# Optimization experiments

Measured on AMD Instinct MI355X. Metric: run time of the kernel, lower is better.

## Reference

```python
import jax, jax.numpy as jnp
import numpy as np

L = 3          # n_layers
B = 512        # batch
H = 1024       # d_model == d_enopt (last-layer hidden is fed back as input)
T = 8          # num_targets
TAU = 96       # decode steps
BETA = 2.0     # softplus beta


def setup_inputs() -> dict:
    key = jax.random.key(0)
    ks = jax.random.split(key, 10)
    s = 0.02
    return {
        "hidden": jax.random.normal(ks[0], (L, B, H), jnp.float32),
        "cell":   jax.random.normal(ks[1], (L, B, H), jnp.float32),
        # stacked per-layer LSTM weights (input size == H for all layers)
        "W_ih": jax.random.normal(ks[2], (L, 4 * H, H), jnp.float32) * s,
        "W_hh": jax.random.normal(ks[3], (L, 4 * H, H), jnp.float32) * s,
        "b_ih": jax.random.normal(ks[4], (L, 4 * H), jnp.float32) * s,
        "b_hh": jax.random.normal(ks[5], (L, 4 * H), jnp.float32) * s,
        "W1": jax.random.normal(ks[6], (T, H), jnp.float32) * s,
        "b1": jax.random.normal(ks[7], (T,), jnp.float32) * s,
        "W2": jax.random.normal(ks[8], (T, H), jnp.float32) * s,
        "b2": jax.random.normal(ks[9], (T,), jnp.float32) * s,
    }


def _lstm_step(h, c, W_ih, W_hh, b_ih, b_hh):
    x = h[-1]  # [B, H]
    new_h, new_c = [], []
    for l in range(L):
        gates = x @ W_ih[l].T + b_ih[l] + h[l] @ W_hh[l].T + b_hh[l]  # [B, 4H]
        i, f, g, o = jnp.split(gates, 4, axis=-1)  # PyTorch gate order i,f,g,o
        i, f, o = jax.nn.sigmoid(i), jax.nn.sigmoid(f), jax.nn.sigmoid(o)
        g = jnp.tanh(g)
        c_l = f * c[l] + i * g
        h_l = o * jnp.tanh(c_l)
        new_h.append(h_l)
        new_c.append(c_l)
        x = h_l  # input to next layer (dropout inactive at inference)
    return jnp.stack(new_h), jnp.stack(new_c), x


def reference(hidden, cell, W_ih, W_hh, b_ih, b_hh, W1, b1, W2, b2):
    def step(carry, _):
        h, c = carry
        h, c, y = _lstm_step(h, c, W_ih, W_hh, b_ih, b_hh)
        return (h, c), y

    (_, _), ys = jax.lax.scan(step, (hidden, cell), None, length=TAU)  # ys: [TAU, B, H]
    out = jnp.transpose(ys, (1, 0, 2))  # [B, TAU, H] (batch_first concat over time)
    mu = out @ W1.T + b1
    sigma = jax.nn.softplus(BETA * (out @ W2.T + b2)) / BETA
    return mu, sigma
```

## Files before the change

kernel.cpp:

```cpp
#include <hip/hip_runtime.h>
#include <hip/hip_bf16.h>
#include <stdint.h>


typedef __attribute__((ext_vector_type(8))) short short8;
typedef __attribute__((ext_vector_type(8))) __bf16 bf16x8_t;
typedef __attribute__((ext_vector_type(4))) float f32x4;
typedef __attribute__((ext_vector_type(4))) unsigned short u16x4;

static __device__ __forceinline__ unsigned short f2bf(float f) {
  unsigned int u = __float_as_uint(f);
  u += 0x7FFFu + ((u >> 16) & 1u);
  return (unsigned short)(u >> 16);
}

static __device__ __forceinline__ float sigm(float x) {
  return 1.0f / (1.0f + __expf(-x));
}
static __device__ __forceinline__ float tanh_f(float x) {
  float xc = fminf(fmaxf(x, -15.f), 15.f);
  float e = __expf(2.0f * xc);
  return 1.0f - 2.0f / (e + 1.0f);
}

static __device__ __forceinline__ void gload_lds16(const void* g, void* l) {
  __builtin_amdgcn_global_load_lds(
      (const __attribute__((address_space(1))) unsigned int*)g,
      (__attribute__((address_space(3))) unsigned int*)l, 16, 0, 0);
}

static __device__ __forceinline__ f32x4 mfma16(short8 a, short8 b, f32x4 c) {
  return __builtin_amdgcn_mfma_f32_16x16x32_bf16((bf16x8_t)a, (bf16x8_t)b, c, 0, 0, 0);
}

__global__ __launch_bounds__(256, 1) void phase_kernel(
    const unsigned short* __restrict__ Wx,
    const unsigned short* __restrict__ xsrc,
    const float* __restrict__ gb_rd,
    float* __restrict__ c_l,
    unsigned short* __restrict__ h_out,
    const float* __restrict__ bias_l,
    int do_proj, int step, float* __restrict__ macc,
    const float* __restrict__ W1, const float* __restrict__ W2,
    const unsigned short* __restrict__ Wh,
    const unsigned short* __restrict__ hsrc,
    float* __restrict__ gb_wr,
    int do_x, int do_h) {
  __shared__ __align__(16) char ldsA[2][32768];

  const int bi = blockIdx.x;
  const int xcd = bi & 7;
  const int rslot = bi >> 3;
  const int pair = xcd * 4 + (rslot >> 3);
  const int mt = rslot & 7;
  const int role = pair & 1;
  const int hcg = pair >> 1;
  const int tile = hcg * 8 + mt;
  const int m0 = mt * 64;
  const int hc0 = hcg * 64;

  if (role == 0) { if (!do_x) return; } else { if (!do_h) return; }

  const unsigned short* A = role ? hsrc : xsrc;
  const unsigned short* W = role ? Wh : Wx;

  const int tid = threadIdx.x;
  const int w = tid >> 6;
  const int lane = tid & 63;
  const int quad = lane >> 4;
  const int l16 = lane & 15;

  const unsigned short* brow[4];
#pragma unroll
  for (int g = 0; g < 4; ++g)
    brow[g] = W + (size_t)(g * 1024 + hc0 + w * 16 + l16) * 1024 + quad * 8;

  const int rbase = tid >> 5;
  const int spos = tid & 31;
  const int wvbase = (tid >> 6) * 1024;

  const int rx0 = l16, rx1 = 16 + l16;

#define STAGE(kc_, buf_)                                                      \
  {                                                                           \
    _Pragma("unroll") for (int j = 0; j < 8; ++j) {                           \
      int r_ = j * 8 + rbase;                                                 \
      int c_ = spos ^ (r_ & 31);                                              \
      gload_lds16(A + (size_t)(m0 + r_) * 1024 + (kc_)*256 + c_ * 8,          \
                  &ldsA[buf_][j * 4096 + wvbase]);                            \
    }                                                                         \
  }

  STAGE(0, 0);
  short8 bfr[4][4];
#pragma unroll
  for (int d = 0; d < 4; ++d)
#pragma unroll
    for (int g = 0; g < 4; ++g) bfr[d][g] = *(const short8*)(brow[g] + d * 32);

  f32x4 acc[4][4];
  if (role == 0) {
#pragma unroll
    for (int mb = 0; mb < 4; ++mb)
#pragma unroll
      for (int g = 0; g < 4; ++g)
        acc[mb][g] = *(const f32x4*)(
            gb_rd + ((size_t)(tile * 4 + w) * 16 + g * 4 + mb) * 256 + lane * 4);
  } else {
    f32x4 z4 = {0.f, 0.f, 0.f, 0.f};
#pragma unroll
    for (int mb = 0; mb < 4; ++mb)
#pragma unroll
      for (int g = 0; g < 4; ++g) acc[mb][g] = z4;
  }
  __syncthreads();

#pragma unroll
  for (int kc = 0; kc < 4; ++kc) {
    if (kc < 3) STAGE(kc + 1, (kc + 1) & 1);
    const char* base = ldsA[kc & 1];
    short8 afr[2][4];
#pragma unroll
    for (int mb = 0; mb < 4; ++mb) {
      int rxm = (mb & 1) ? rx1 : rx0;
      afr[0][mb] =
          *(const short8*)(base + (mb * 16 + l16) * 512 + ((quad ^ rxm) << 4));
    }
#pragma unroll
    for (int ks = 0; ks < 8; ++ks) {
      const int kg = kc * 8 + ks;
      short8 a0 = afr[ks & 1][0], a1 = afr[ks & 1][1];
      short8 a2 = afr[ks & 1][2], a3 = afr[ks & 1][3];
      short8 b0 = bfr[kg & 3][0], b1 = bfr[kg & 3][1];
      short8 b2 = bfr[kg & 3][2], b3 = bfr[kg & 3][3];
      if (ks < 7) {
#pragma unroll
        for (int mb = 0; mb < 4; ++mb) {
          int rxm = (mb & 1) ? rx1 : rx0;
          afr[(ks + 1) & 1][mb] =
              *(const short8*)(base + (mb * 16 + l16) * 512 +
                               ((((ks + 1) * 4 + quad) ^ rxm) << 4));
        }
      }
      if (kg + 4 < 32) {
#pragma unroll
        for (int g = 0; g < 4; ++g)
          bfr[kg & 3][g] = *(const short8*)(brow[g] + (kg + 4) * 32);
      }
      acc[0][0] = mfma16(a0, b0, acc[0][0]);
      acc[1][0] = mfma16(a1, b0, acc[1][0]);
      acc[2][0] = mfma16(a2, b0, acc[2][0]);
      acc[3][0] = mfma16(a3, b0, acc[3][0]);
      acc[0][1] = mfma16(a0, b1, acc[0][1]);
      acc[1][1] = mfma16(a1, b1, acc[1][1]);
      acc[2][1] = mfma16(a2, b1, acc[2][1]);
      acc[3][1] = mfma16(a3, b1, acc[3][1]);
      acc[0][2] = mfma16(a0, b2, acc[0][2]);
      acc[1][2] = mfma16(a1, b2, acc[1][2]);
      acc[2][2] = mfma16(a2, b2, acc[2][2]);
      acc[3][2] = mfma16(a3, b2, acc[3][2]);
      acc[0][3] = mfma16(a0, b3, acc[0][3]);
      acc[1][3] = mfma16(a1, b3, acc[1][3]);
      acc[2][3] = mfma16(a2, b3, acc[2][3]);
      acc[3][3] = mfma16(a3, b3, acc[3][3]);
    }
    if (kc < 3) __syncthreads();
  }
#undef STAGE

  if (role == 1) {
#pragma unroll
    for (int mb = 0; mb < 4; ++mb)
#pragma unroll
      for (int g = 0; g < 4; ++g)
        *(f32x4*)(gb_wr + ((size_t)(tile * 4 + w) * 16 + g * 4 + mb) * 256 +
                  lane * 4) = acc[mb][g];
    return;
  }

  const int colh = hc0 + w * 16 + l16;
  float bs0 = bias_l[colh];
  float bs1 = bias_l[1024 + colh];
  float bs2 = bias_l[2048 + colh];
  float bs3 = bias_l[3072 + colh];
  float hv[16];
#pragma unroll
  for (int mb = 0; mb < 4; ++mb) {
#pragma unroll
    for (int rr = 0; rr < 4; ++rr) {
      int row = m0 + mb * 16 + quad * 4 + rr;
      float gi = acc[mb][0][rr] + bs0;
      float gf = acc[mb][1][rr] + bs1;
      float gg = acc[mb][2][rr] + bs2;
      float go = acc[mb][3][rr] + bs3;
      float* cp = c_l + (size_t)row * 1024 + colh;
      float cn = sigm(gf) * (*cp) + sigm(gi) * tanh_f(gg);
      *cp = cn;
      float h = sigm(go) * tanh_f(cn);
      hv[mb * 4 + rr] = h;
      h_out[(size_t)row * 1024 + colh] = f2bf(h);
    }
  }

  if (do_proj) {
    float* hbuf = (float*)ldsA[0];
    float* projred = (float*)ldsA[1];
#pragma unroll
    for (int mb = 0; mb < 4; ++mb)
#pragma unroll
      for (int rr = 0; rr < 4; ++rr)
        hbuf[(mb * 16 + quad * 4 + rr) * 65 + w * 16 + l16] = hv[mb * 4 + rr];
    __syncthreads();

    const int m = tid & 63;
    const int grp = tid >> 6;
    float pm[8], ps[8];
    float hj[16];
#pragma unroll
    for (int j = 0; j < 16; ++j) hj[j] = hbuf[m * 65 + grp * 16 + j];
#pragma unroll
    for (int t = 0; t < 8; ++t) {
      const f32x4* w1p = (const f32x4*)(W1 + t * 1024 + hc0 + grp * 16);
      const f32x4* w2p = (const f32x4*)(W2 + t * 1024 + hc0 + grp * 16);
      float s1 = 0.f, s2 = 0.f;
#pragma unroll
      for (int v = 0; v < 4; ++v) {
        f32x4 wa = w1p[v], wb = w2p[v];
#pragma unroll
        for (int j = 0; j < 4; ++j) {
          s1 += hj[v * 4 + j] * wa[j];
          s2 += hj[v * 4 + j] * wb[j];
        }
      }
      pm[t] = s1;
      ps[t] = s2;
    }
#pragma unroll
    for (int t = 0; t < 8; ++t) {
      projred[(grp * 64 + m) * 17 + t] = pm[t];
      projred[(grp * 64 + m) * 17 + 8 + t] = ps[t];
    }
    __syncthreads();
#pragma unroll
    for (int q = 0; q < 4; ++q) {
      int s = grp * 4 + q;
      float v = projred[m * 17 + s] + projred[(64 + m) * 17 + s] +
                projred[(128 + m) * 17 + s] + projred[(192 + m) * 17 + s];
      atomicAdd(&macc[((size_t)(m0 + m) * 96 + step) * 16 + s], v);
    }
  }
}

__global__ void conv_w(const f32x4* __restrict__ wi, const f32x4* __restrict__ wh,
                       u16x4* __restrict__ wib, u16x4* __restrict__ whb) {
  int i = blockIdx.x * 256 + threadIdx.x;
  f32x4 a = wi[i], b = wh[i];
  u16x4 pa, pb;
#pragma unroll
  for (int j = 0; j < 4; ++j) {
    pa[j] = f2bf(a[j]);
    pb[j] = f2bf(b[j]);
  }
  wib[i] = pa;
  whb[i] = pb;
}

__global__ void init_state(const f32x4* __restrict__ hid, const f32x4* __restrict__ cel,
                           const f32x4* __restrict__ bih, const f32x4* __restrict__ bhh,
                           u16x4* __restrict__ hb, f32x4* __restrict__ cs,
                           f32x4* __restrict__ bias) {
  int i = blockIdx.x * 256 + threadIdx.x;
  f32x4 h = hid[i];
  u16x4 p;
#pragma unroll
  for (int j = 0; j < 4; ++j) p[j] = f2bf(h[j]);
  hb[i] = p;
  cs[i] = cel[i];
  if (i < 3072) bias[i] = bih[i] + bhh[i];
}

__global__ void finalize_k(const float* __restrict__ macc, const float* __restrict__ b1,
                           const float* __restrict__ b2, float* __restrict__ out) {
  int idx = blockIdx.x * 256 + threadIdx.x;
  int t = idx & 7;
  int bt = idx >> 3;
  float mu = macc[bt * 16 + t] + b1[t];
  float z2 = 2.0f * (macc[bt * 16 + 8 + t] + b2[t]);
  float sp = fmaxf(z2, 0.f) + log1pf(__expf(-fabsf(z2)));
  out[idx] = mu;
  out[393216 + idx] = 0.5f * sp;
}

extern "C" void kernel_launch(void* const* d_in, const int* in_sizes, int n_in,
                              void* d_out, int out_size, void* d_ws, size_t ws_size,
                              hipStream_t stream) {
  (void)in_sizes; (void)n_in; (void)out_size; (void)ws_size;
  const float* hidden = (const float*)d_in[0];
  const float* cell = (const float*)d_in[1];
  const float* Wih = (const float*)d_in[2];
  const float* Whh = (const float*)d_in[3];
  const float* bih = (const float*)d_in[4];
  const float* bhh = (const float*)d_in[5];
  const float* W1 = (const float*)d_in[6];
  const float* b1 = (const float*)d_in[7];
  const float* W2 = (const float*)d_in[8];
  const float* b2 = (const float*)d_in[9];
  float* out = (float*)d_out;

  char* ws = (char*)d_ws;
  unsigned short* Wih_b = (unsigned short*)(ws);
  unsigned short* Whh_b = (unsigned short*)(ws + 25165824);
  unsigned short* h_b = (unsigned short*)(ws + 50331648);
  float* c_s = (float*)(ws + 53477376);
  float* gbuf = (float*)(ws + 59768832);
  float* bias = (float*)(ws + 84934656);
  float* macc = (float*)(ws + 84983808);

  hipMemsetAsync(macc, 0, 3145728, stream);
  conv_w<<<12288, 256, 0, stream>>>((const f32x4*)Wih, (const f32x4*)Whh,
                                    (u16x4*)Wih_b, (u16x4*)Whh_b);
  init_state<<<1536, 256, 0, stream>>>((const f32x4*)hidden, (const f32x4*)cell,
                                       (const f32x4*)bih, (const f32x4*)bhh,
                                       (u16x4*)h_b, (f32x4*)c_s, (f32x4*)bias);

  phase_kernel<<<256, 256, 0, stream>>>(Wih_b, h_b, gbuf, c_s, h_b, bias, 0, 0,
                                        macc, W1, W2, Whh_b, h_b, gbuf,
                                        0, 1);

  for (int t = 0; t < 96; ++t) {
    for (int l = 0; l < 3; ++l) {
      int lh = (l + 1) % 3;
      int do_h = (t == 95 && l == 2) ? 0 : 1;
      const unsigned short* xsrc =
          h_b + (size_t)((l == 0) ? 2 : (l - 1)) * 524288;
      phase_kernel<<<256, 256, 0, stream>>>(
          Wih_b + (size_t)l * 4194304, xsrc, gbuf + (size_t)l * 2097152,
          c_s + (size_t)l * 524288, h_b + (size_t)l * 524288, bias + l * 4096,
          (l == 2) ? 1 : 0, t, macc, W1, W2, Whh_b + (size_t)lh * 4194304,
          h_b + (size_t)lh * 524288, gbuf + (size_t)lh * 2097152, 1,
          do_h);
    }
  }
  finalize_k<<<1536, 256, 0, stream>>>(macc, b1, b2, out);
}
```

Before: 9.694 ms.

## Fuse per-phase launches into one persistent kernel with grid barrier

Replaces 289 separate phase_kernel launches with a single persistent kernel that loops over all phases internally. Blocks synchronize between phases with an atomic-counter grid barrier. The aim is to remove kernel launch overhead and the inter-kernel gaps. It relies on all 256 blocks being co-resident, and the spin barrier adds its own latency to every phase.

```diff
diff --git a/kernel.cpp b/kernel.cpp
--- a/kernel.cpp
+++ b/kernel.cpp
@@ -1,5 +1,4 @@
 #include <hip/hip_runtime.h>
-#include <hip/hip_bf16.h>
 #include <stdint.h>
 
 
@@ -33,19 +32,16 @@
   return __builtin_amdgcn_mfma_f32_16x16x32_bf16((bf16x8_t)a, (bf16x8_t)b, c, 0, 0, 0);
 }
 
-__global__ __launch_bounds__(256, 1) void phase_kernel(
-    const unsigned short* __restrict__ Wx,
-    const unsigned short* __restrict__ xsrc,
-    const float* __restrict__ gb_rd,
-    float* __restrict__ c_l,
-    unsigned short* __restrict__ h_out,
-    const float* __restrict__ bias_l,
-    int do_proj, int step, float* __restrict__ macc,
+__global__ __launch_bounds__(256, 1) void persist_kernel(
+    const unsigned short* __restrict__ WihA,
+    const unsigned short* __restrict__ WhhA,
+    unsigned short* __restrict__ hB,
+    float* __restrict__ cS,
+    float* __restrict__ gB,
+    const float* __restrict__ biasA,
+    float* __restrict__ macc,
     const float* __restrict__ W1, const float* __restrict__ W2,
-    const unsigned short* __restrict__ Wh,
-    const unsigned short* __restrict__ hsrc,
-    float* __restrict__ gb_wr,
-    int do_x, int do_h) {
+    unsigned* __restrict__ bar) {
   __shared__ __align__(16) char ldsA[2][32768];
 
   const int bi = blockIdx.x;
@@ -59,26 +55,14 @@
   const int m0 = mt * 64;
   const int hc0 = hcg * 64;
 
-  if (role == 0) { if (!do_x) return; } else { if (!do_h) return; }
-
-  const unsigned short* A = role ? hsrc : xsrc;
-  const unsigned short* W = role ? Wh : Wx;
-
   const int tid = threadIdx.x;
   const int w = tid >> 6;
   const int lane = tid & 63;
   const int quad = lane >> 4;
   const int l16 = lane & 15;
-
-  const unsigned short* brow[4];
-#pragma unroll
-  for (int g = 0; g < 4; ++g)
-    brow[g] = W + (size_t)(g * 1024 + hc0 + w * 16 + l16) * 1024 + quad * 8;
-
   const int rbase = tid >> 5;
   const int spos = tid & 31;
-  const int wvbase = (tid >> 6) * 1024;
-
+  const int wvbase = w * 1024;
   const int rx0 = l16, rx1 = 16 + l16;
 
 #define STAGE(kc_, buf_)                                                      \
@@ -86,169 +70,216 @@
     _Pragma("unroll") for (int j = 0; j < 8; ++j) {                           \
       int r_ = j * 8 + rbase;                                                 \
       int c_ = spos ^ (r_ & 31);                                              \
-      gload_lds16(A + (size_t)(m0 + r_) * 1024 + (kc_)*256 + c_ * 8,          \
+      gload_lds16(Ap + (size_t)(m0 + r_) * 1024 + (kc_)*256 + c_ * 8,         \
                   &ldsA[buf_][j * 4096 + wvbase]);                            \
     }                                                                         \
   }
 
-  STAGE(0, 0);
-  short8 bfr[4][4];
-#pragma unroll
-  for (int d = 0; d < 4; ++d)
-#pragma unroll
-    for (int g = 0; g < 4; ++g) bfr[d][g] = *(const short8*)(brow[g] + d * 32);
-
-  f32x4 acc[4][4];
-  if (role == 0) {
-#pragma unroll
-    for (int mb = 0; mb < 4; ++mb)
+#pragma unroll 1
+  for (int p = 0; p < 289; ++p) {
+    const int l = (p == 0) ? 2 : (p - 1) % 3;
+    const int st = (p == 0) ? 0 : (p - 1) / 3;
+    const int lh = (l + 1) % 3;
+    const int do_x = (p != 0);
+    const int do_h = (p != 288);
+    const int do_proj = (p != 0) && (l == 2);
+    const int active = role ? do_h : do_x;
+
+    if (active) {
+      const unsigned short* Wp;
+      const unsigned short* Ap;
+      if (role) {
+        Wp = WhhA + (size_t)lh * 4194304;
+        Ap = hB + (size_t)lh * 524288;
+      } else {
+        Wp = WihA + (size_t)l * 4194304;
+        Ap = hB + (size_t)((l == 0) ? 2 : (l - 1)) * 524288;
+      }
+
+      const unsigned short* brow[4];
 #pragma unroll
       for (int g = 0; g < 4; ++g)
-        acc[mb][g] = *(const f32x4*)(
-            gb_rd + ((size_t)(tile * 4 + w) * 16 + g * 4 + mb) * 256 + lane * 4);
-  } else {
-    f32x4 z4 = {0.f, 0.f, 0.f, 0.f};
-#pragma unroll
-    for (int mb = 0; mb < 4; ++mb)
-#pragma unroll
-      for (int g = 0; g < 4; ++g) acc[mb][g] = z4;
-  }
-  __syncthreads();
-
-#pragma unroll
-  for (int kc = 0; kc < 4; ++kc) {
-    if (kc < 3) STAGE(kc + 1, (kc + 1) & 1);
-    const char* base = ldsA[kc & 1];
-    short8 afr[2][4];
-#pragma unroll
-    for (int mb = 0; mb < 4; ++mb) {
-      int rxm = (mb & 1) ? rx1 : rx0;
-      afr[0][mb] =
-          *(const short8*)(base + (mb * 16 + l16) * 512 + ((quad ^ rxm) << 4));
-    }
-#pragma unroll
-    for (int ks = 0; ks < 8; ++ks) {
-      const int kg = kc * 8 + ks;
-      short8 a0 = afr[ks & 1][0], a1 = afr[ks & 1][1];
-      short8 a2 = afr[ks & 1][2], a3 = afr[ks & 1][3];
-      short8 b0 = bfr[kg & 3][0], b1 = bfr[kg & 3][1];
-      short8 b2 = bfr[kg & 3][2], b3 = bfr[kg & 3][3];
-      if (ks < 7) {
+        brow[g] = Wp + (size_t)(g * 1024 + hc0 + w * 16 + l16) * 1024 + quad * 8;
+
+      STAGE(0, 0);
+      short8 bfr[4][4];
+#pragma unroll
+      for (int d = 0; d < 4; ++d)
+#pragma unroll
+        for (int g = 0; g < 4; ++g) bfr[d][g] = *(const short8*)(brow[g] + d * 32);
+
+      f32x4 acc[4][4];
+      if (role == 0) {
+        const float* gb_rd = gB + (size_t)l * 2097152;
+#pragma unroll
+        for (int mb = 0; mb < 4; ++mb)
+#pragma unroll
+          for (int g = 0; g < 4; ++g)
+            acc[mb][g] = *(const f32x4*)(
+                gb_rd + ((size_t)(tile * 4 + w) * 16 + g * 4 + mb) * 256 + lane * 4);
+      } else {
+        f32x4 z4 = {0.f, 0.f, 0.f, 0.f};
+#pragma unroll
+        for (int mb = 0; mb < 4; ++mb)
+#pragma unroll
+          for (int g = 0; g < 4; ++g) acc[mb][g] = z4;
+      }
+      __syncthreads();
+
+#pragma unroll
+      for (int kc = 0; kc < 4; ++kc) {
+        if (kc < 3) STAGE(kc + 1, (kc + 1) & 1);
+        const char* base = ldsA[kc & 1];
+        short8 afr[2][4];
 #pragma unroll
         for (int mb = 0; mb < 4; ++mb) {
           int rxm = (mb & 1) ? rx1 : rx0;
-          afr[(ks + 1) & 1][mb] =
-              *(const short8*)(base + (mb * 16 + l16) * 512 +
-                               ((((ks + 1) * 4 + quad) ^ rxm) << 4));
+          afr[0][mb] =
+              *(const short8*)(base + (mb * 16 + l16) * 512 + ((quad ^ rxm) << 4));
         }
-      }
-      if (kg + 4 < 32) {
-#pragma unroll
-        for (int g = 0; g < 4; ++g)
-          bfr[kg & 3][g] = *(const short8*)(brow[g] + (kg + 4) * 32);
-      }
-      acc[0][0] = mfma16(a0, b0, acc[0][0]);
-      acc[1][0] = mfma16(a1, b0, acc[1][0]);
-      acc[2][0] = mfma16(a2, b0, acc[2][0]);
-      acc[3][0] = mfma16(a3, b0, acc[3][0]);
-      acc[0][1] = mfma16(a0, b1, acc[0][1]);
-      acc[1][1] = mfma16(a1, b1, acc[1][1]);
-      acc[2][1] = mfma16(a2, b1, acc[2][1]);
-      acc[3][1] = mfma16(a3, b1, acc[3][1]);
-      acc[0][2] = mfma16(a0, b2, acc[0][2]);
-      acc[1][2] = mfma16(a1, b2, acc[1][2]);
-      acc[2][2] = mfma16(a2, b2, acc[2][2]);
-      acc[3][2] = mfma16(a3, b2, acc[3][2]);
-      acc[0][3] = mfma16(a0, b3, acc[0][3]);
-      acc[1][3] = mfma16(a1, b3, acc[1][3]);
-      acc[2][3] = mfma16(a2, b3, acc[2][3]);
-      acc[3][3] = mfma16(a3, b3, acc[3][3]);
+#pragma unroll
+        for (int ks = 0; ks < 8; ++ks) {
+          const int kg = kc * 8 + ks;
+          short8 a0 = afr[ks & 1][0], a1 = afr[ks & 1][1];
+          short8 a2 = afr[ks & 1][2], a3 = afr[ks & 1][3];
+          short8 b0 = bfr[kg & 3][0], b1 = bfr[kg & 3][1];
+          short8 b2 = bfr[kg & 3][2], b3 = bfr[kg & 3][3];
+          if (ks < 7) {
+#pragma unroll
+            for (int mb = 0; mb < 4; ++mb) {
+              int rxm = (mb & 1) ? rx1 : rx0;
+              afr[(ks + 1) & 1][mb] =
+                  *(const short8*)(base + (mb * 16 + l16) * 512 +
+                                   ((((ks + 1) * 4 + quad) ^ rxm) << 4));
+            }
+          }
+          if (kg + 4 < 32) {
+#pragma unroll
+            for (int g = 0; g < 4; ++g)
+              bfr[kg & 3][g] = *(const short8*)(brow[g] + (kg + 4) * 32);
+          }
+          acc[0][0] = mfma16(a0, b0, acc[0][0]);
+          acc[1][0] = mfma16(a1, b0, acc[1][0]);
+          acc[2][0] = mfma16(a2, b0, acc[2][0]);
+          acc[3][0] = mfma16(a3, b0, acc[3][0]);
+          acc[0][1] = mfma16(a0, b1, acc[0][1]);
+          acc[1][1] = mfma16(a1, b1, acc[1][1]);
+          acc[2][1] = mfma16(a2, b1, acc[2][1]);
+          acc[3][1] = mfma16(a3, b1, acc[3][1]);
+          acc[0][2] = mfma16(a0, b2, acc[0][2]);
+          acc[1][2] = mfma16(a1, b2, acc[1][2]);
+          acc[2][2] = mfma16(a2, b2, acc[2][2]);
+          acc[3][2] = mfma16(a3, b2, acc[3][2]);
+          acc[0][3] = mfma16(a0, b3, acc[0][3]);
+          acc[1][3] = mfma16(a1, b3, acc[1][3]);
+          acc[2][3] = mfma16(a2, b3, acc[2][3]);
+          acc[3][3] = mfma16(a3, b3, acc[3][3]);
+        }
+        if (kc < 3) __syncthreads();
+      }
+
+      if (role == 1) {
+        float* gb_wr = gB + (size_t)lh * 2097152;
+#pragma unroll
+        for (int mb = 0; mb < 4; ++mb)
+#pragma unroll
+          for (int g = 0; g < 4; ++g)
+            *(f32x4*)(gb_wr + ((size_t)(tile * 4 + w) * 16 + g * 4 + mb) * 256 +
+                      lane * 4) = acc[mb][g];
+      } else {
+        float* c_l = cS + (size_t)l * 524288;
+        unsigned short* h_out = hB + (size_t)l * 524288;
+        const float* bias_l = biasA + l * 4096;
+        const int colh = hc0 + w * 16 + l16;
+        float bs0 = bias_l[colh];
+        float bs1 = bias_l[1024 + colh];
+        float bs2 = bias_l[2048 + colh];
+        float bs3 = bias_l[3072 + colh];
+        float hv[16];
+#pragma unroll
+        for (int mb = 0; mb < 4; ++mb) {
+#pragma unroll
+          for (int rr = 0; rr < 4; ++rr) {
+            int row = m0 + mb * 16 + quad * 4 + rr;
+            float gi = acc[mb][0][rr] + bs0;
+            float gf = acc[mb][1][rr] + bs1;
+            float gg = acc[mb][2][rr] + bs2;
+            float go = acc[mb][3][rr] + bs3;
+            float* cp = c_l + (size_t)row * 1024 + colh;
+            float cn = sigm(gf) * (*cp) + sigm(gi) * tanh_f(gg);
+            *cp = cn;
+            float h = sigm(go) * tanh_f(cn);
+            hv[mb * 4 + rr] = h;
+            h_out[(size_t)row * 1024 + colh] = f2bf(h);
+          }
+        }
+
+        if (do_proj) {
+          float* hbuf = (float*)ldsA[0];
+          float* projred = (float*)ldsA[1];
+#pragma unroll
+          for (int mb = 0; mb < 4; ++mb)
+#pragma unroll
+            for (int rr = 0; rr < 4; ++rr)
+              hbuf[(mb * 16 + quad * 4 + rr) * 65 + w * 16 + l16] = hv[mb * 4 + rr];
+          __syncthreads();
+
+          const int m = tid & 63;
+          const int grp = tid >> 6;
+          float pm[8], ps[8];
+          float hj[16];
+#pragma unroll
+          for (int j = 0; j < 16; ++j) hj[j] = hbuf[m * 65 + grp * 16 + j];
+#pragma unroll
+          for (int tt = 0; tt < 8; ++tt) {
+            const f32x4* w1p = (const f32x4*)(W1 + tt * 1024 + hc0 + grp * 16);
+            const f32x4* w2p = (const f32x4*)(W2 + tt * 1024 + hc0 + grp * 16);
+            float s1 = 0.f, s2 = 0.f;
+#pragma unroll
+            for (int v = 0; v < 4; ++v) {
+              f32x4 wa = w1p[v], wb = w2p[v];
+#pragma unroll
+              for (int j = 0; j < 4; ++j) {
+                s1 += hj[v * 4 + j] * wa[j];
+                s2 += hj[v * 4 + j] * wb[j];
+              }
+            }
+            pm[tt] = s1;
+            ps[tt] = s2;
+          }
+#pragma unroll
+          for (int tt = 0; tt < 8; ++tt) {
+            projred[(grp * 64 + m) * 17 + tt] = pm[tt];
+            projred[(grp * 64 + m) * 17 + 8 + tt] = ps[tt];
+          }
+          __syncthreads();
+#pragma unroll
+          for (int q = 0; q < 4; ++q) {
+            int s = grp * 4 + q;
+            float v = projred[m * 17 + s] + projred[(64 + m) * 17 + s] +
+                      projred[(128 + m) * 17 + s] + projred[(192 + m) * 17 + s];
+            atomicAdd(&macc[((size_t)(m0 + m) * 96 + st) * 16 + s], v);
+          }
+        }
+      }
     }
-    if (kc < 3) __syncthreads();
+
+    if (p < 288) {
+      __syncthreads();
+      if (tid == 0) {
+        __threadfence();
+        __hip_atomic_fetch_add(bar, 1u, __ATOMIC_RELAXED,
+                               __HIP_MEMORY_SCOPE_AGENT);
+        const unsigned tgt = 256u * (unsigned)(p + 1);
+        while (__hip_atomic_load(bar, __ATOMIC_RELAXED,
+                                 __HIP_MEMORY_SCOPE_AGENT) < tgt)
+          __builtin_amdgcn_s_sleep(1);
+        __threadfence();
+      }
+      __syncthreads();
+    }
   }
 #undef STAGE
-
-  if (role == 1) {
-#pragma unroll
-    for (int mb = 0; mb < 4; ++mb)
-#pragma unroll
-      for (int g = 0; g < 4; ++g)
-        *(f32x4*)(gb_wr + ((size_t)(tile * 4 + w) * 16 + g * 4 + mb) * 256 +
-                  lane * 4) = acc[mb][g];
-    return;
-  }
-
-  const int colh = hc0 + w * 16 + l16;
-  float bs0 = bias_l[colh];
-  float bs1 = bias_l[1024 + colh];
-  float bs2 = bias_l[2048 + colh];
-  float bs3 = bias_l[3072 + colh];
-  float hv[16];
-#pragma unroll
-  for (int mb = 0; mb < 4; ++mb) {
-#pragma unroll
-    for (int rr = 0; rr < 4; ++rr) {
-      int row = m0 + mb * 16 + quad * 4 + rr;
-      float gi = acc[mb][0][rr] + bs0;
-      float gf = acc[mb][1][rr] + bs1;
-      float gg = acc[mb][2][rr] + bs2;
-      float go = acc[mb][3][rr] + bs3;
-      float* cp = c_l + (size_t)row * 1024 + colh;
-      float cn = sigm(gf) * (*cp) + sigm(gi) * tanh_f(gg);
-      *cp = cn;
-      float h = sigm(go) * tanh_f(cn);
-      hv[mb * 4 + rr] = h;
-      h_out[(size_t)row * 1024 + colh] = f2bf(h);
-    }
-  }
-
-  if (do_proj) {
-    float* hbuf = (float*)ldsA[0];
-    float* projred = (float*)ldsA[1];
-#pragma unroll
-    for (int mb = 0; mb < 4; ++mb)
-#pragma unroll
-      for (int rr = 0; rr < 4; ++rr)
-        hbuf[(mb * 16 + quad * 4 + rr) * 65 + w * 16 + l16] = hv[mb * 4 + rr];
-    __syncthreads();
-
-    const int m = tid & 63;
-    const int grp = tid >> 6;
-    float pm[8], ps[8];
-    float hj[16];
-#pragma unroll
-    for (int j = 0; j < 16; ++j) hj[j] = hbuf[m * 65 + grp * 16 + j];
-#pragma unroll
-    for (int t = 0; t < 8; ++t) {
-      const f32x4* w1p = (const f32x4*)(W1 + t * 1024 + hc0 + grp * 16);
-      const f32x4* w2p = (const f32x4*)(W2 + t * 1024 + hc0 + grp * 16);
-      float s1 = 0.f, s2 = 0.f;
-#pragma unroll
-      for (int v = 0; v < 4; ++v) {
-        f32x4 wa = w1p[v], wb = w2p[v];
-#pragma unroll
-        for (int j = 0; j < 4; ++j) {
-          s1 += hj[v * 4 + j] * wa[j];
-          s2 += hj[v * 4 + j] * wb[j];
-        }
-      }
-      pm[t] = s1;
-      ps[t] = s2;
-    }
-#pragma unroll
-    for (int t = 0; t < 8; ++t) {
-      projred[(grp * 64 + m) * 17 + t] = pm[t];
-      projred[(grp * 64 + m) * 17 + 8 + t] = ps[t];
-    }
-    __syncthreads();
-#pragma unroll
-    for (int q = 0; q < 4; ++q) {
-      int s = grp * 4 + q;
-      float v = projred[m * 17 + s] + projred[(64 + m) * 17 + s] +
-                projred[(128 + m) * 17 + s] + projred[(192 + m) * 17 + s];
-      atomicAdd(&macc[((size_t)(m0 + m) * 96 + step) * 16 + s], v);
-    }
-  }
 }
 
 __global__ void conv_w(const f32x4* __restrict__ wi, const f32x4* __restrict__ wh,
@@ -315,31 +346,18 @@
   float* gbuf = (float*)(ws + 59768832);
   float* bias = (float*)(ws + 84934656);
   float* macc = (float*)(ws + 84983808);
+  unsigned* bar = (unsigned*)(ws + 88129536);
 
   hipMemsetAsync(macc, 0, 3145728, stream);
+  hipMemsetAsync(bar, 0, 64, stream);
   conv_w<<<12288, 256, 0, stream>>>((const f32x4*)Wih, (const f32x4*)Whh,
                                     (u16x4*)Wih_b, (u16x4*)Whh_b);
   init_state<<<1536, 256, 0, stream>>>((const f32x4*)hidden, (const f32x4*)cell,
                                        (const f32x4*)bih, (const f32x4*)bhh,
                                        (u16x4*)h_b, (f32x4*)c_s, (f32x4*)bias);
 
-  phase_kernel<<<256, 256, 0, stream>>>(Wih_b, h_b, gbuf, c_s, h_b, bias, 0, 0,
-                                        macc, W1, W2, Whh_b, h_b, gbuf,
-                                        0, 1);
-
-  for (int t = 0; t < 96; ++t) {
-    for (int l = 0; l < 3; ++l) {
-      int lh = (l + 1) % 3;
-      int do_h = (t == 95 && l == 2) ? 0 : 1;
-      const unsigned short* xsrc =
-          h_b + (size_t)((l == 0) ? 2 : (l - 1)) * 524288;
-      phase_kernel<<<256, 256, 0, stream>>>(
-          Wih_b + (size_t)l * 4194304, xsrc, gbuf + (size_t)l * 2097152,
-          c_s + (size_t)l * 524288, h_b + (size_t)l * 524288, bias + l * 4096,
-          (l == 2) ? 1 : 0, t, macc, W1, W2, Whh_b + (size_t)lh * 4194304,
-          h_b + (size_t)lh * 524288, gbuf + (size_t)lh * 2097152, 1,
-          do_h);
-    }
-  }
+  persist_kernel<<<256, 256, 0, stream>>>(Wih_b, Whh_b, h_b, c_s, gbuf, bias,
+                                          macc, W1, W2, bar);
+
   finalize_k<<<1536, 256, 0, stream>>>(macc, b1, b2, out);
 }
```

Measured after the change: 15.00 ms. 1.55x slower.
